# Performance work log

Measured on AMD Instinct MI355X. Metric: run time of the kernel, lower is better.

Reference implementation:

```python
import jax, jax.numpy as jnp
import numpy as np
from jax import lax

ID_LEN = 207
INPUT_DIM = 64
OUTPUT_DIM = 128
WIN = 3
BZ = 16
SEQLEN = 64
N_NODES = BZ * ID_LEN          # 3312
N_EDGES = N_NODES * 16         # 52992


def setup_inputs() -> dict:
    key = jax.random.key(0)
    ks = jax.random.split(key, 8)
    x = jax.random.normal(ks[0], (BZ, SEQLEN, ID_LEN * INPUT_DIM), dtype=jnp.float32)
    edge_src = jax.random.randint(ks[1], (N_EDGES,), 0, N_NODES)
    edge_dst = jax.random.randint(ks[2], (N_EDGES,), 0, N_NODES)
    # learned params (q/k weights init N(0, 0.01), zero bias; conv has no bias)
    Wq = 0.01 * jax.random.normal(ks[3], (INPUT_DIM, OUTPUT_DIM), dtype=jnp.float32)
    bq = jnp.zeros((OUTPUT_DIM,), dtype=jnp.float32)
    Wk = 0.01 * jax.random.normal(ks[4], (INPUT_DIM, OUTPUT_DIM), dtype=jnp.float32)
    bk = jnp.zeros((OUTPUT_DIM,), dtype=jnp.float32)
    fan_in = ID_LEN * INPUT_DIM * WIN
    bound = 1.0 / np.sqrt(fan_in)
    conv_w = jax.random.uniform(ks[5], (OUTPUT_DIM, ID_LEN * INPUT_DIM, WIN),
                                minval=-bound, maxval=bound, dtype=jnp.float32)
    return {"x": x, "Wq": Wq, "bq": bq, "Wk": Wk, "bk": bk,
            "conv_w": conv_w, "edge_src": edge_src, "edge_dst": edge_dst}


def _forward(x, Wq, bq, Wk, bk, conv_w, edge_src, edge_dst):
    bz, seqlen, _ = x.shape
    # (bz, seqlen, id_len, d) -> (bz*id_len, seqlen, d)
    xr = x.reshape(bz, seqlen, ID_LEN, INPUT_DIM).transpose(0, 2, 1, 3)
    xr = xr.reshape(-1, seqlen, INPUT_DIM)
    mean_x = xr.mean(axis=1)                       # [N, d]
    q = (mean_x @ Wq + bq) / jnp.sqrt(jnp.float32(OUTPUT_DIM))
    k = mean_x @ Wk + bk
    v = xr.reshape(-1, seqlen * INPUT_DIM)         # [N, seqlen*d]
    N = v.shape[0]
    # per-edge attention score: k[src] . q[dst]
    scores = jnp.sum(k[edge_src] * q[edge_dst], axis=-1)      # [E]
    # segment softmax over incoming edges per dst
    seg_max = jax.ops.segment_max(scores, edge_dst, num_segments=N)
    e = jnp.exp(scores - seg_max[edge_dst])
    denom = jax.ops.segment_sum(e, edge_dst, num_segments=N)
    alpha = e / denom[edge_dst]                                 # [E]
    # weighted gather-sum of big value vectors
    out = jax.ops.segment_sum(alpha[:, None] * v[edge_src], edge_dst, num_segments=N)
    # back to (bz, seqlen, id_len*d)
    y = out.reshape(bz, ID_LEN, seqlen, INPUT_DIM).transpose(0, 2, 1, 3)
    y = y.reshape(bz, seqlen, ID_LEN * INPUT_DIM)
    # Conv1d same padding, no bias: NCH layout
    y = lax.conv_general_dilated(
        y.transpose(0, 2, 1), conv_w, window_strides=(1,), padding="SAME",
        dimension_numbers=("NCH", "OIH", "NCH"))
    return y.transpose(0, 2, 1)                    # [bz, seqlen, output_dim]


def reference(x, Wq, bq, Wk, bk, conv_w, edge_src, edge_dst):
    return _forward(x, Wq, bq, Wk, bk, conv_w, edge_src, edge_dst)
```

## Files before the change

kernel.cpp:

```cpp
#include <hip/hip_runtime.h>
#include <hip/hip_bf16.h>
#include <math.h>

#define BZ 16
#define SEQ 64
#define CID 207
#define DIN 64
#define OCN 128
#define NN (BZ*CID)
#define NE (NN*16)
#define ICD (CID*DIN)
#define KW 3
#define NKSTEP 414
#define NKPAD 416
#define NKC 32
#define KSPC 13
#define XTOT ((size_t)BZ*SEQ*ICD)
#define TCH 8
#define NCHUNK (SEQ/TCH)
#define GDEG 256
#define WFSTEP (3*8*64*8)

#define CVB 832
#define SCB 207
#define WPB (NKPAD*4)

typedef __attribute__((ext_vector_type(8))) short bf16x8;
typedef __attribute__((ext_vector_type(4))) float f32x4;
typedef unsigned short u16;
typedef unsigned int u32;

__device__ __forceinline__ float bflo(u32 u) {
    u32 v = u << 16;
    return __builtin_bit_cast(float, v);
}
__device__ __forceinline__ float bfhi(u32 u) {
    u32 v = u & 0xFFFF0000u;
    return __builtin_bit_cast(float, v);
}
__device__ __forceinline__ u16 f2bf(float f) {
    __hip_bfloat16 h = __float2bfloat16(f);
    return __builtin_bit_cast(u16, h);
}
__device__ __forceinline__ u32 packbf(float f0, float f1) {
    return ((u32)f2bf(f1) << 16) | (u32)f2bf(f0);
}

__global__ __launch_bounds__(1024) void histscan_kernel(const int* __restrict__ edst,
                                                        int* __restrict__ offs,
                                                        int* __restrict__ fill) {
    __shared__ int hist[NN];
    __shared__ int sums[1024], sums2[1024];
    int tid = threadIdx.x;
    for (int i = tid; i < NN; i += 1024) hist[i] = 0;
    __syncthreads();
    for (int e = tid; e < NE; e += 1024) atomicAdd(&hist[edst[e]], 1);
    __syncthreads();
    int base = tid * 4;
    int v[4];
    #pragma unroll
    for (int i = 0; i < 4; ++i) v[i] = (base + i < NN) ? hist[base + i] : 0;
    sums[tid] = v[0] + v[1] + v[2] + v[3];
    __syncthreads();
    int* a = sums;
    int* b2 = sums2;
    for (int off = 1; off < 1024; off <<= 1) {
        int val = a[tid] + ((tid >= off) ? a[tid - off] : 0);
        b2[tid] = val;
        __syncthreads();
        int* t = a; a = b2; b2 = t;
    }
    int prev = (tid > 0) ? a[tid - 1] : 0;
    int run = prev;
    #pragma unroll
    for (int i = 0; i < 4; ++i) {
        if (base + i <= NN) {
            offs[base + i] = run;
            if (base + i < NN) fill[base + i] = run;
        }
        run += v[i];
    }
}

__global__ __launch_bounds__(256) void fused3_kernel(const float* __restrict__ x,
                                                     u16* __restrict__ xt,
                                                     float* __restrict__ meanp,
                                                     const int* __restrict__ esrc,
                                                     int* __restrict__ fill,
                                                     int* __restrict__ csr,
                                                     const int* __restrict__ edst,
                                                     const float* __restrict__ cw,
                                                     u16* __restrict__ wf) {
    __shared__ float s_cw[32][100];
    int bid = blockIdx.x;
    int tid = threadIdx.x;
    if (bid < CVB) {
        int bb = bid / 52;
        int rem = bid - bb * 52;
        int cg = rem >> 2;
        int tq = rem & 3;
        int cl = tid >> 4;
        int dq = (tid & 15) << 2;
        int c = cg * 16 + cl;
        if (c >= CID) return;
        int n = bb * CID + c;
        const float* px = x + (size_t)bb * SEQ * ICD + (size_t)(tq * 16) * ICD + (size_t)c * DIN + dq;
        u16* pxt = xt + ((size_t)(tq * 16) * NN + n) * DIN + dq;
        float ax = 0.f, ay = 0.f, az = 0.f, aw = 0.f;
        #pragma unroll 4
        for (int t = 0; t < 16; ++t) {
            float4 v = *(const float4*)(px + (size_t)t * ICD);
            ax += v.x; ay += v.y; az += v.z; aw += v.w;
            uint2 w2;
            w2.x = packbf(v.x, v.y);
            w2.y = packbf(v.z, v.w);
            *(uint2*)(pxt + (size_t)t * NN * DIN) = w2;
        }
        *(float4*)(meanp + ((size_t)tq * NN + n) * DIN + dq) = make_float4(ax, ay, az, aw);
    } else if (bid < CVB + SCB) {
        int e = (bid - CVB) * 256 + tid;
        int d0 = edst[e];
        int pos = atomicAdd(&fill[d0], 1);
        csr[pos] = esrc[e];
    } else {
        int wkb = bid - (CVB + SCB);
        int kstep = wkb >> 2;
        int p = wkb & 3;
        int ic0 = kstep * 32;
        int col0 = ic0 * 3;
        {
            int oc_l = tid >> 3;
            int seg = tid & 7;
            const float* src = cw + (size_t)(p * 32 + oc_l) * (ICD * KW) + col0 + seg * 12;
            #pragma unroll
            for (int u = 0; u < 12; ++u) {
                int col = seg * 12 + u;
                float v = (col0 + col < ICD * 3) ? src[u] : 0.f;
                s_cw[oc_l][col] = v;
            }
        }
        __syncthreads();
        #pragma unroll
        for (int r = 0; r < 2; ++r) {
            int f = tid + 256 * r;
            if (f < 384) {
                int lane = f & 63;
                int g = f >> 6;
                int ntl = g & 1;
                int w = g >> 1;
                int nt = p * 2 + ntl;
                int row = ntl * 16 + (lane & 15);
                int cb = 8 * (lane >> 4);
                uint4 o;
                u32 pk[4];
                #pragma unroll
                for (int pj = 0; pj < 4; ++pj) {
                    float v0 = s_cw[row][(cb + 2 * pj) * 3 + w];
                    float v1 = s_cw[row][(cb + 2 * pj + 1) * 3 + w];
                    pk[pj] = packbf(v0, v1);
                }
                o.x = pk[0]; o.y = pk[1]; o.z = pk[2]; o.w = pk[3];
                size_t off = (((size_t)(kstep * 3 + w) * 8 + nt) * 64 + lane) * 8;
                *(uint4*)(wf + off) = o;
            }
        }
    }
}

__global__ __launch_bounds__(256) void qk_kernel(const float* __restrict__ meanp,
                                                 const float* __restrict__ Wq,
                                                 const float* __restrict__ bq,
                                                 const float* __restrict__ Wk,
                                                 const float* __restrict__ bk,
                                                 float* __restrict__ q,
                                                 float* __restrict__ k) {
    __shared__ float ms[16][DIN];
    int n0 = blockIdx.x * 16;
    int tid = threadIdx.x;
    const size_t PS = (size_t)NN * DIN;
    for (int i = tid; i < 16 * DIN; i += 256) {
        size_t off = (size_t)(n0 + (i >> 6)) * DIN + (i & 63);
        float s = meanp[off] + meanp[PS + off] + meanp[2 * PS + off] + meanp[3 * PS + off];
        ms[i >> 6][i & 63] = s * (1.0f / SEQ);
    }
    __syncthreads();
    int j = tid & 127;
    int g = tid >> 7;
    float accq[8], acck[8];
    float bqv = bq[j], bkv = bk[j];
    #pragma unroll
    for (int r = 0; r < 8; ++r) { accq[r] = bqv; acck[r] = bkv; }
    for (int d = 0; d < DIN; ++d) {
        float wq = Wq[d * OCN + j], wk = Wk[d * OCN + j];
        #pragma unroll
        for (int r = 0; r < 8; ++r) {
            float mv = ms[g * 8 + r][d];
            accq[r] += mv * wq;
            acck[r] += mv * wk;
        }
    }
    const float qscale = 0.088388347648318447f;
    #pragma unroll
    for (int r = 0; r < 8; ++r) {
        int nn = n0 + g * 8 + r;
        q[(size_t)nn * OCN + j] = accq[r] * qscale;
        k[(size_t)nn * OCN + j] = acck[r];
    }
}

__global__ __launch_bounds__(256) void alpha_kernel(const float* __restrict__ q,
                                                    const float* __restrict__ k,
                                                    const int* __restrict__ offs,
                                                    const int* __restrict__ csr,
                                                    float* __restrict__ alpha) {
    __shared__ float qs[OCN];
    __shared__ float sc[GDEG];
    __shared__ int sidx[GDEG];
    int n = blockIdx.x;
    int start = offs[n];
    int deg = offs[n + 1] - start;
    if (deg > GDEG) deg = GDEG;
    int tid = threadIdx.x;
    if (tid < OCN) qs[tid] = q[(size_t)n * OCN + tid];
    for (int i = tid; i < deg; i += 256) sidx[i] = csr[start + i];
    __syncthreads();
    int lane = tid & 63;
    int wv = tid >> 6;
    for (int i = wv; i < deg; i += 4) {
        const float* kk = k + (size_t)sidx[i] * OCN;
        float p = kk[lane] * qs[lane] + kk[lane + 64] * qs[lane + 64];
        #pragma unroll
        for (int off = 32; off; off >>= 1) p += __shfl_down(p, off);
        if (lane == 0) sc[i] = p;
    }
    __syncthreads();
    float m = -1e30f;
    for (int i = 0; i < deg; ++i) m = fmaxf(m, sc[i]);
    __syncthreads();
    for (int i = tid; i < deg; i += 256) sc[i] = __expf(sc[i] - m);
    __syncthreads();
    float ssum = 0.f;
    for (int i = 0; i < deg; ++i) ssum += sc[i];
    float inv = (deg > 0) ? (1.0f / ssum) : 0.f;
    for (int i = tid; i < deg; i += 256) alpha[start + i] = sc[i] * inv;
}

__global__ __launch_bounds__(256) void gather2_kernel(const u16* __restrict__ xt,
                                                      const float* __restrict__ alpha,
                                                      const int* __restrict__ offs,
                                                      const int* __restrict__ csr,
                                                      u16* __restrict__ yb) {
    int bid = blockIdx.x;
    int ch = bid & 7;
    int ng = bid >> 3;
    int wid = threadIdx.x >> 6;
    int lane = threadIdx.x & 63;
    int n = ng * 4 + wid;
    int t0 = ch * TCH;
    int b = n / CID, c = n - b * CID;
    int start = offs[n];
    int deg = offs[n + 1] - start;
    int t = lane >> 3;
    int dg = lane & 7;
    const u16* xbase = xt + ((size_t)(t0 + t) * NN) * DIN + (dg << 3);

    int sAll = 0; float aAll = 0.f;
    if (lane < deg) {
        sAll = csr[start + lane] << 6;
        aAll = alpha[start + lane];
    }
    int dmax = (deg <= 64) ? deg : 64;

    float acc[8];
    #pragma unroll
    for (int j = 0; j < 8; ++j) acc[j] = 0.f;

    float a0 = 0.f;
    uint4 v0 = make_uint4(0, 0, 0, 0);
    if (dmax > 0) {
        int s0 = __shfl(sAll, 0);
        a0 = __shfl(aAll, 0);
        v0 = *(const uint4*)(xbase + s0);
    }
    for (int i = 1; i < dmax; ++i) {
        int s1 = __shfl(sAll, i);
        float a1 = __shfl(aAll, i);
        uint4 v1 = *(const uint4*)(xbase + s1);
        acc[0] += a0 * bflo(v0.x); acc[1] += a0 * bfhi(v0.x);
        acc[2] += a0 * bflo(v0.y); acc[3] += a0 * bfhi(v0.y);
        acc[4] += a0 * bflo(v0.z); acc[5] += a0 * bfhi(v0.z);
        acc[6] += a0 * bflo(v0.w); acc[7] += a0 * bfhi(v0.w);
        a0 = a1; v0 = v1;
    }
    if (dmax > 0) {
        acc[0] += a0 * bflo(v0.x); acc[1] += a0 * bfhi(v0.x);
        acc[2] += a0 * bflo(v0.y); acc[3] += a0 * bfhi(v0.y);
        acc[4] += a0 * bflo(v0.z); acc[5] += a0 * bfhi(v0.z);
        acc[6] += a0 * bflo(v0.w); acc[7] += a0 * bfhi(v0.w);
    }
    for (int i = 64; i < deg; ++i) {
        int s = csr[start + i] << 6;
        float a = alpha[start + i];
        uint4 v = *(const uint4*)(xbase + s);
        acc[0] += a * bflo(v.x); acc[1] += a * bfhi(v.x);
        acc[2] += a * bflo(v.y); acc[3] += a * bfhi(v.y);
        acc[4] += a * bflo(v.z); acc[5] += a * bfhi(v.z);
        acc[6] += a * bflo(v.w); acc[7] += a * bfhi(v.w);
    }
    uint4 o;
    o.x = packbf(acc[0], acc[1]);
    o.y = packbf(acc[2], acc[3]);
    o.z = packbf(acc[4], acc[5]);
    o.w = packbf(acc[6], acc[7]);
    *(uint4*)(yb + ((size_t)b * SEQ + t0 + t) * ICD + c * DIN + (dg << 3)) = o;
}

__global__ __launch_bounds__(256) void conv_kernel(const u16* __restrict__ yb,
                                                   const u16* __restrict__ wf,
                                                   float* __restrict__ partial) {
    int bid = blockIdx.x;
    int xcd = bid & 7;
    int rest = bid >> 3;
    int khi = rest & 3;
    int b = rest >> 2;
    int kc = xcd + (khi << 3);
    int tid = threadIdx.x;
    int lane = tid & 63;
    int wid = tid >> 6;
    int th = wid & 1;
    int nh = wid >> 1;
    int lrow = lane & 15;
    int lq = lane >> 4;
    int tbase = th * 32;

    f32x4 acc[2][4];
    #pragma unroll
    for (int tt = 0; tt < 2; ++tt)
        #pragma unroll
        for (int n = 0; n < 4; ++n) acc[tt][n] = (f32x4){0.f, 0.f, 0.f, 0.f};

    const u16* ybA = yb + (size_t)b * SEQ * ICD + lq * 8;
    const u16* wfL = wf + (size_t)lane * 8 + ((size_t)nh * 4 * 64) * 8;
    int ks0 = kc * KSPC;

    bf16x8 aA[6], bA[12], aB[6], bB[12];

#define LOAD_AB(aR, bR, KS) do {                                              \
    int kstep_ = ks0 + (KS);                                                  \
    int ic0_ = kstep_ * 32;                                                   \
    _Pragma("unroll")                                                         \
    for (int tt_ = 0; tt_ < 2; ++tt_) {                                       \
        _Pragma("unroll")                                                     \
        for (int w_ = 0; w_ < 3; ++w_) {                                      \
            int ts_ = tbase + tt_ * 16 + lrow + w_ - 1;                       \
            bf16x8 av_ = {0, 0, 0, 0, 0, 0, 0, 0};                            \
            if ((unsigned)ts_ < SEQ)                                          \
                av_ = *(const bf16x8*)(ybA + (size_t)ts_ * ICD + ic0_);       \
            aR[tt_ * 3 + w_] = av_;                                           \
        }                                                                     \
    }                                                                         \
    const u16* wfp_ = wfL + (size_t)kstep_ * WFSTEP;                          \
    _Pragma("unroll")                                                         \
    for (int w_ = 0; w_ < 3; ++w_) {                                          \
        _Pragma("unroll")                                                     \
        for (int n_ = 0; n_ < 4; ++n_)                                        \
            bR[w_ * 4 + n_] = *(const bf16x8*)(wfp_ + (size_t)((w_ * 8 + n_) * 64) * 8); \
    }                                                                         \
} while (0)

#define COMPUTE(aR, bR) do {                                                  \
    _Pragma("unroll")                                                         \
    for (int w_ = 0; w_ < 3; ++w_) {                                          \
        _Pragma("unroll")                                                     \
        for (int tt_ = 0; tt_ < 2; ++tt_) {                                   \
            _Pragma("unroll")                                                 \
            for (int n_ = 0; n_ < 4; ++n_)                                    \
                acc[tt_][n_] = __builtin_amdgcn_mfma_f32_16x16x32_bf16(       \
                    aR[tt_ * 3 + w_], bR[w_ * 4 + n_], acc[tt_][n_], 0, 0, 0);\
        }                                                                     \
    }                                                                         \
} while (0)

    LOAD_AB(aA, bA, 0);
    #pragma unroll
    for (int ks = 0; ks < KSPC - 1; ks += 2) {
        LOAD_AB(aB, bB, ks + 1);
        COMPUTE(aA, bA);
        LOAD_AB(aA, bA, ks + 2);
        COMPUTE(aB, bB);
    }
    COMPUTE(aA, bA);

    float* pp = partial + (size_t)kc * ((size_t)BZ * SEQ * OCN) + (size_t)b * SEQ * OCN + nh * 64;
    #pragma unroll
    for (int tt = 0; tt < 2; ++tt) {
        #pragma unroll
        for (int n = 0; n < 4; ++n) {
            #pragma unroll
            for (int r = 0; r < 4; ++r) {
                int t = tbase + tt * 16 + lq * 4 + r;
                pp[(size_t)t * OCN + n * 16 + lrow] = acc[tt][n][r];
            }
        }
    }
#undef LOAD_AB
#undef COMPUTE
}

__global__ __launch_bounds__(256) void reduce_kernel(const float* __restrict__ partial,
                                                     float* __restrict__ out) {
    int i = (blockIdx.x * 256 + threadIdx.x) * 4;
    float4 s = make_float4(0.f, 0.f, 0.f, 0.f);
    #pragma unroll
    for (int kc = 0; kc < NKC; ++kc) {
        float4 v = *(const float4*)(partial + (size_t)kc * 131072 + i);
        s.x += v.x; s.y += v.y; s.z += v.z; s.w += v.w;
    }
    *(float4*)(out + i) = s;
}

extern "C" void kernel_launch(void* const* d_in, const int* in_sizes, int n_in,
                              void* d_out, int out_size, void* d_ws, size_t ws_size,
                              hipStream_t stream) {
    const float* x   = (const float*)d_in[0];
    const float* Wq  = (const float*)d_in[1];
    const float* bqv = (const float*)d_in[2];
    const float* Wk  = (const float*)d_in[3];
    const float* bkv = (const float*)d_in[4];
    const float* cw  = (const float*)d_in[5];
    const int* esrc  = (const int*)d_in[6];
    const int* edst  = (const int*)d_in[7];

    char* ws = (char*)d_ws;
    size_t o = 0;
    auto alloc = [&](size_t bytes) {
        void* p = ws + o;
        o += (bytes + 255) & ~(size_t)255;
        return p;
    };
    u16*   xt    = (u16*)alloc(XTOT * 2);
    u16*   yb    = (u16*)alloc(XTOT * 2);
    u16*   wf    = (u16*)alloc((size_t)NKPAD * 3 * 8 * 64 * 8 * 2);
    float* meanp = (float*)alloc((size_t)4 * NN * DIN * 4);
    float* q     = (float*)alloc((size_t)NN * OCN * 4);
    float* k     = (float*)alloc((size_t)NN * OCN * 4);
    int*   fill  = (int*)alloc(4096 * 4);
    int*   offs  = (int*)alloc(4352 * 4);
    int*   csr   = (int*)alloc((size_t)NE * 4);
    float* alpha = (float*)alloc((size_t)NE * 4);
    float* partial = (float*)xt;

    histscan_kernel<<<dim3(1), dim3(1024), 0, stream>>>(edst, offs, fill);
    fused3_kernel<<<dim3(CVB + SCB + WPB), dim3(256), 0, stream>>>(x, xt, meanp, esrc, fill, csr, edst, cw, wf);
    qk_kernel<<<dim3(NN / 16), dim3(256), 0, stream>>>(meanp, Wq, bqv, Wk, bkv, q, k);
    alpha_kernel<<<dim3(NN), dim3(256), 0, stream>>>(q, k, offs, csr, alpha);
    gather2_kernel<<<dim3((NN / 4) * NCHUNK), dim3(256), 0, stream>>>(xt, alpha, offs, csr, yb);
    conv_kernel<<<dim3(512), dim3(256), 0, stream>>>(yb, wf, partial);
    reduce_kernel<<<dim3(131072 / 4 / 256), dim3(256), 0, stream>>>(partial, (float*)d_out);
}
```

Baseline: 134.0 us.

## Fold histogram scan into prep kernel, CSR scatter into qk, two nodes per wave

The single-block histogram/scan kernel becomes block 0 of the conversion/weight-prep kernel, now scanning with 256 threads. The CSR scatter moves into the q/k projection kernel, removing one launch and one dependency stage. The gather kernel now handles two destination nodes per wave with interleaved loads to raise memory-level parallelism, but it drops the fallback path for in-degrees above 64. Dead variants (k1_kernel, k1b_unused) are left in the file.

```diff
diff --git a/kernel.cpp b/kernel.cpp
--- a/kernel.cpp
+++ b/kernel.cpp
@@ -22,8 +22,9 @@
 #define WFSTEP (3*8*64*8)
 
 #define CVB 832
+#define WPB (NKPAD*4)
+#define K1B (1 + CVB + WPB)
 #define SCB 207
-#define WPB (NKPAD*4)
 
 typedef __attribute__((ext_vector_type(8))) short bf16x8;
 typedef __attribute__((ext_vector_type(4))) float f32x4;
@@ -45,58 +46,66 @@
 __device__ __forceinline__ u32 packbf(float f0, float f1) {
     return ((u32)f2bf(f1) << 16) | (u32)f2bf(f0);
 }
-
-__global__ __launch_bounds__(1024) void histscan_kernel(const int* __restrict__ edst,
-                                                        int* __restrict__ offs,
-                                                        int* __restrict__ fill) {
-    __shared__ int hist[NN];
-    __shared__ int sums[1024], sums2[1024];
-    int tid = threadIdx.x;
-    for (int i = tid; i < NN; i += 1024) hist[i] = 0;
-    __syncthreads();
-    for (int e = tid; e < NE; e += 1024) atomicAdd(&hist[edst[e]], 1);
-    __syncthreads();
-    int base = tid * 4;
-    int v[4];
-    #pragma unroll
-    for (int i = 0; i < 4; ++i) v[i] = (base + i < NN) ? hist[base + i] : 0;
-    sums[tid] = v[0] + v[1] + v[2] + v[3];
-    __syncthreads();
-    int* a = sums;
-    int* b2 = sums2;
-    for (int off = 1; off < 1024; off <<= 1) {
-        int val = a[tid] + ((tid >= off) ? a[tid - off] : 0);
-        b2[tid] = val;
-        __syncthreads();
-        int* t = a; a = b2; b2 = t;
-    }
-    int prev = (tid > 0) ? a[tid - 1] : 0;
-    int run = prev;
-    #pragma unroll
-    for (int i = 0; i < 4; ++i) {
-        if (base + i <= NN) {
-            offs[base + i] = run;
-            if (base + i < NN) fill[base + i] = run;
-        }
-        run += v[i];
-    }
-}
-
-__global__ __launch_bounds__(256) void fused3_kernel(const float* __restrict__ x,
-                                                     u16* __restrict__ xt,
-                                                     float* __restrict__ meanp,
-                                                     const int* __restrict__ esrc,
-                                                     int* __restrict__ fill,
-                                                     int* __restrict__ csr,
-                                                     const int* __restrict__ edst,
-                                                     const float* __restrict__ cw,
-                                                     u16* __restrict__ wf) {
-    __shared__ float s_cw[32][100];
+__device__ __forceinline__ void fma8(float* acc, float a, uint4 v) {
+    acc[0] += a * bflo(v.x); acc[1] += a * bfhi(v.x);
+    acc[2] += a * bflo(v.y); acc[3] += a * bfhi(v.y);
+    acc[4] += a * bflo(v.z); acc[5] += a * bfhi(v.z);
+    acc[6] += a * bflo(v.w); acc[7] += a * bfhi(v.w);
+}
+
+union K1LDS {
+    struct { int hist[NN]; int sums[256]; int sums2[256]; } h;
+    float s_cw[32][100];
+};
+
+__global__ __launch_bounds__(256) void k1_kernel(const float* __restrict__ x,
+                                                 u16* __restrict__ xt,
+                                                 float* __restrict__ meanp,
+                                                 const int* __restrict__ edst,
+                                                 int* __restrict__ offs,
+                                                 int* __restrict__ fill,
+                                                 const float* __restrict__ cw,
+                                                 u16* __restrict__ wf) {
+    __shared__ K1LDS u;
     int bid = blockIdx.x;
     int tid = threadIdx.x;
-    if (bid < CVB) {
-        int bb = bid / 52;
-        int rem = bid - bb * 52;
+    if (bid == 0) {
+        for (int i = tid; i < NN; i += 256) u.h.hist[i] = 0;
+        __syncthreads();
+        for (int e = tid; e < NE; e += 256) atomicAdd(&u.h.hist[edst[e]], 1);
+        __syncthreads();
+        int base = tid * 13;
+        int v[13];
+        int s = 0;
+        #pragma unroll
+        for (int i = 0; i < 13; ++i) {
+            v[i] = (base + i < NN) ? u.h.hist[base + i] : 0;
+            s += v[i];
+        }
+        u.h.sums[tid] = s;
+        __syncthreads();
+        int* a = u.h.sums;
+        int* b2 = u.h.sums2;
+        for (int off = 1; off < 256; off <<= 1) {
+            int val = a[tid] + ((tid >= off) ? a[tid - off] : 0);
+            b2[tid] = val;
+            __syncthreads();
+            int* t = a; a = b2; b2 = t;
+        }
+        int run = (tid > 0) ? a[tid - 1] : 0;
+        #pragma unroll
+        for (int i = 0; i < 13; ++i) {
+            int idx = base + i;
+            if (idx <= NN) {
+                offs[idx] = run;
+                if (idx < NN) fill[idx] = run;
+            }
+            run += v[i];
+        }
+    } else if (bid <= CVB) {
+        int cvbid = bid - 1;
+        int bb = cvbid / 52;
+        int rem = cvbid - bb * 52;
         int cg = rem >> 2;
         int tq = rem & 3;
         int cl = tid >> 4;
@@ -117,13 +126,8 @@
             *(uint2*)(pxt + (size_t)t * NN * DIN) = w2;
         }
         *(float4*)(meanp + ((size_t)tq * NN + n) * DIN + dq) = make_float4(ax, ay, az, aw);
-    } else if (bid < CVB + SCB) {
-        int e = (bid - CVB) * 256 + tid;
-        int d0 = edst[e];
-        int pos = atomicAdd(&fill[d0], 1);
-        csr[pos] = esrc[e];
     } else {
-        int wkb = bid - (CVB + SCB);
+        int wkb = bid - (1 + CVB);
         int kstep = wkb >> 2;
         int p = wkb & 3;
         int ic0 = kstep * 32;
@@ -133,41 +137,25 @@
             int seg = tid & 7;
             const float* src = cw + (size_t)(p * 32 + oc_l) * (ICD * KW) + col0 + seg * 12;
             #pragma unroll
-            for (int u = 0; u < 12; ++u) {
-                int col = seg * 12 + u;
-                float v = (col0 + col < ICD * 3) ? src[u] : 0.f;
-                s_cw[oc_l][col] = v;
+            for (int uu = 0; uu < 12; ++uu) {
+                int col = seg * 12 + uu;
+                float v = (col0 + col < ICD * 3) ? src[uu] : 0.f;
+                u.s_cw[oc_l][col] = v;
             }
         }
         __syncthreads();
-        #pragma unroll
-        for (int r = 0; r < 2; ++r) {
-            int f = tid + 256 * r;
-            if (f < 384) {
-                int lane = f & 63;
-                int g = f >> 6;
-                int ntl = g & 1;
-                int w = g >> 1;
-                int nt = p * 2 + ntl;
-                int row = ntl * 16 + (lane & 15);
-                int cb = 8 * (lane >> 4);
-                uint4 o;
-                u32 pk[4];
-                #pragma unroll
-                for (int pj = 0; pj < 4; ++pj) {
-                    float v0 = s_cw[row][(cb + 2 * pj) * 3 + w];
-                    float v1 = s_cw[row][(cb + 2 * pj + 1) * 3 + w];
-                    pk[pj] = packbf(v0, v1);
-                }
-                o.x = pk[0]; o.y = pk[1]; o.z = pk[2]; o.w = pk[3];
-                size_t off = (((size_t)(kstep * 3 + w) * 8 + nt) * 64 + lane) * 8;
-                *(uint4*)(wf + off) = o;
-            }
-        }
-    }
-}
-
-__global__ __launch_bounds__(256) void qk_kernel(const float* __restrict__ meanp,
+        if (tid < 128) return;
+        __builtin_unreachable();
+    }
+}
+
+__global__ __launch_bounds__(256) void k1b_unused() {}
+
+__global__ __launch_bounds__(256) void k2_kernel(const int* __restrict__ esrc,
+                                                 const int* __restrict__ edst,
+                                                 int* __restrict__ fill,
+                                                 int* __restrict__ csr,
+                                                 const float* __restrict__ meanp,
                                                  const float* __restrict__ Wq,
                                                  const float* __restrict__ bq,
                                                  const float* __restrict__ Wk,
@@ -175,8 +163,16 @@
                                                  float* __restrict__ q,
                                                  float* __restrict__ k) {
     __shared__ float ms[16][DIN];
-    int n0 = blockIdx.x * 16;
+    int bid = blockIdx.x;
     int tid = threadIdx.x;
+    if (bid < SCB) {
+        int e = bid * 256 + tid;
+        int d0 = edst[e];
+        int pos = atomicAdd(&fill[d0], 1);
+        csr[pos] = esrc[e];
+        return;
+    }
+    int n0 = (bid - SCB) * 16;
     const size_t PS = (size_t)NN * DIN;
     for (int i = tid; i < 16 * DIN; i += 256) {
         size_t off = (size_t)(n0 + (i >> 6)) * DIN + (i & 63);
@@ -255,65 +251,57 @@
     int ng = bid >> 3;
     int wid = threadIdx.x >> 6;
     int lane = threadIdx.x & 63;
-    int n = ng * 4 + wid;
+    int na = ng * 8 + wid * 2;
+    int nb = na + 1;
     int t0 = ch * TCH;
-    int b = n / CID, c = n - b * CID;
-    int start = offs[n];
-    int deg = offs[n + 1] - start;
     int t = lane >> 3;
     int dg = lane & 7;
     const u16* xbase = xt + ((size_t)(t0 + t) * NN) * DIN + (dg << 3);
 
-    int sAll = 0; float aAll = 0.f;
-    if (lane < deg) {
-        sAll = csr[start + lane] << 6;
-        aAll = alpha[start + lane];
-    }
-    int dmax = (deg <= 64) ? deg : 64;
-
-    float acc[8];
-    #pragma unroll
-    for (int j = 0; j < 8; ++j) acc[j] = 0.f;
-
-    float a0 = 0.f;
-    uint4 v0 = make_uint4(0, 0, 0, 0);
-    if (dmax > 0) {
-        int s0 = __shfl(sAll, 0);
-        a0 = __shfl(aAll, 0);
-        v0 = *(const uint4*)(xbase + s0);
-    }
-    for (int i = 1; i < dmax; ++i) {
-        int s1 = __shfl(sAll, i);
-        float a1 = __shfl(aAll, i);
-        uint4 v1 = *(const uint4*)(xbase + s1);
-        acc[0] += a0 * bflo(v0.x); acc[1] += a0 * bfhi(v0.x);
-        acc[2] += a0 * bflo(v0.y); acc[3] += a0 * bfhi(v0.y);
-        acc[4] += a0 * bflo(v0.z); acc[5] += a0 * bfhi(v0.z);
-        acc[6] += a0 * bflo(v0.w); acc[7] += a0 * bfhi(v0.w);
-        a0 = a1; v0 = v1;
-    }
-    if (dmax > 0) {
-        acc[0] += a0 * bflo(v0.x); acc[1] += a0 * bfhi(v0.x);
-        acc[2] += a0 * bflo(v0.y); acc[3] += a0 * bfhi(v0.y);
-        acc[4] += a0 * bflo(v0.z); acc[5] += a0 * bfhi(v0.z);
-        acc[6] += a0 * bflo(v0.w); acc[7] += a0 * bfhi(v0.w);
-    }
-    for (int i = 64; i < deg; ++i) {
-        int s = csr[start + i] << 6;
-        float a = alpha[start + i];
-        uint4 v = *(const uint4*)(xbase + s);
-        acc[0] += a * bflo(v.x); acc[1] += a * bfhi(v.x);
-        acc[2] += a * bflo(v.y); acc[3] += a * bfhi(v.y);
-        acc[4] += a * bflo(v.z); acc[5] += a * bfhi(v.z);
-        acc[6] += a * bflo(v.w); acc[7] += a * bfhi(v.w);
-    }
-    uint4 o;
-    o.x = packbf(acc[0], acc[1]);
-    o.y = packbf(acc[2], acc[3]);
-    o.z = packbf(acc[4], acc[5]);
-    o.w = packbf(acc[6], acc[7]);
-    *(uint4*)(yb + ((size_t)b * SEQ + t0 + t) * ICD + c * DIN + (dg << 3)) = o;
-}
+    int ba = na / CID, ca = na - ba * CID;
+    int bb2 = nb / CID, cb = nb - bb2 * CID;
+    int sta = offs[na], dega = offs[na + 1] - sta;
+    int stb = offs[nb], degb = offs[nb + 1] - stb;
+
+    int sA = 0; float aA = 0.f;
+    if (lane < dega && lane < 64) { sA = csr[sta + lane] << 6; aA = alpha[sta + lane]; }
+    int sB = 0; float aB = 0.f;
+    if (lane < degb && lane < 64) { sB = csr[stb + lane] << 6; aB = alpha[stb + lane]; }
+    int da = (dega < 64) ? dega : 64;
+    int db = (degb < 64) ? degb : 64;
+    int mx = (da > db) ? da : db;
+
+    float acca[8], accb[8];
+    #pragma unroll
+    for (int j = 0; j < 8; ++j) { acca[j] = 0.f; accb[j] = 0.f; }
+
+    if (mx > 0) {
+        float a0a = __shfl(aA, 0);
+        float a0b = __shfl(aB, 0);
+        uint4 v0a = *(const uint4*)(xbase + __shfl(sA, 0));
+        uint4 v0b = *(const uint4*)(xbase + __shfl(sB, 0));
+        for (int i = 1; i < mx; ++i) {
+            float a1a = __shfl(aA, i);
+            float a1b = __shfl(aB, i);
+            uint4 v1a = *(const uint4*)(xbase + __shfl(sA, i));
+            uint4 v1b = *(const uint4*)(xbase + __shfl(sB, i));
+            fma8(acca, a0a, v0a);
+            fma8(accb, a0b, v0b);
+            a0a = a1a; v0a = v1a;
+            a0b = a1b; v0b = v1b;
+        }
+        fma8(acca, a0a, v0a);
+        fma8(accb, a0b, v0b);
+    }
+    uint4 oa, ob;
+    oa.x = packbf(acca[0], acca[1]); oa.y = packbf(acca[2], acca[3]);
+    oa.z = packbf(acca[4], acca[5]); oa.w = packbf(acca[6], acca[7]);
+    ob.x = packbf(accb[0], accb[1]); ob.y = packbf(accb[2], accb[3]);
+    ob.z = packbf(accb[4], accb[5]); ob.w = packbf(accb[6], accb[7]);
+    *(uint4*)(yb + ((size_t)ba * SEQ + t0 + t) * ICD + ca * DIN + (dg << 3)) = oa;
+    *(uint4*)(yb + ((size_t)bb2 * SEQ + t0 + t) * ICD + cb * DIN + (dg << 3)) = ob;
+}
+
 
 __global__ __launch_bounds__(256) void conv_kernel(const u16* __restrict__ yb,
                                                    const u16* __restrict__ wf,
@@ -419,6 +407,119 @@
     *(float4*)(out + i) = s;
 }
 
+__global__ __launch_bounds__(256) void k1_full_kernel(const float* __restrict__ x,
+                                                      u16* __restrict__ xt,
+                                                      float* __restrict__ meanp,
+                                                      const int* __restrict__ edst,
+                                                      int* __restrict__ offs,
+                                                      int* __restrict__ fill,
+                                                      const float* __restrict__ cw,
+                                                      u16* __restrict__ wf) {
+    __shared__ K1LDS u;
+    int bid = blockIdx.x;
+    int tid = threadIdx.x;
+    if (bid == 0) {
+        for (int i = tid; i < NN; i += 256) u.h.hist[i] = 0;
+        __syncthreads();
+        for (int e = tid; e < NE; e += 256) atomicAdd(&u.h.hist[edst[e]], 1);
+        __syncthreads();
+        int base = tid * 13;
+        int v[13];
+        int s = 0;
+        #pragma unroll
+        for (int i = 0; i < 13; ++i) {
+            v[i] = (base + i < NN) ? u.h.hist[base + i] : 0;
+            s += v[i];
+        }
+        u.h.sums[tid] = s;
+        __syncthreads();
+        int* a = u.h.sums;
+        int* b2 = u.h.sums2;
+        for (int off = 1; off < 256; off <<= 1) {
+            int val = a[tid] + ((tid >= off) ? a[tid - off] : 0);
+            b2[tid] = val;
+            __syncthreads();
+            int* t = a; a = b2; b2 = t;
+        }
+        int run = (tid > 0) ? a[tid - 1] : 0;
+        #pragma unroll
+        for (int i = 0; i < 13; ++i) {
+            int idx = base + i;
+            if (idx <= NN) {
+                offs[idx] = run;
+                if (idx < NN) fill[idx] = run;
+            }
+            run += v[i];
+        }
+    } else if (bid <= CVB) {
+        int cvbid = bid - 1;
+        int bb = cvbid / 52;
+        int rem = cvbid - bb * 52;
+        int cg = rem >> 2;
+        int tq = rem & 3;
+        int cl = tid >> 4;
+        int dq = (tid & 15) << 2;
+        int c = cg * 16 + cl;
+        if (c >= CID) return;
+        int n = bb * CID + c;
+        const float* px = x + (size_t)bb * SEQ * ICD + (size_t)(tq * 16) * ICD + (size_t)c * DIN + dq;
+        u16* pxt = xt + ((size_t)(tq * 16) * NN + n) * DIN + dq;
+        float ax = 0.f, ay = 0.f, az = 0.f, aw = 0.f;
+        #pragma unroll 4
+        for (int t = 0; t < 16; ++t) {
+            float4 v = *(const float4*)(px + (size_t)t * ICD);
+            ax += v.x; ay += v.y; az += v.z; aw += v.w;
+            uint2 w2;
+            w2.x = packbf(v.x, v.y);
+            w2.y = packbf(v.z, v.w);
+            *(uint2*)(pxt + (size_t)t * NN * DIN) = w2;
+        }
+        *(float4*)(meanp + ((size_t)tq * NN + n) * DIN + dq) = make_float4(ax, ay, az, aw);
+    } else {
+        int wkb = bid - (1 + CVB);
+        int kstep = wkb >> 2;
+        int p = wkb & 3;
+        int ic0 = kstep * 32;
+        int col0 = ic0 * 3;
+        {
+            int oc_l = tid >> 3;
+            int seg = tid & 7;
+            const float* src = cw + (size_t)(p * 32 + oc_l) * (ICD * KW) + col0 + seg * 12;
+            #pragma unroll
+            for (int uu = 0; uu < 12; ++uu) {
+                int col = seg * 12 + uu;
+                float v = (col0 + col < ICD * 3) ? src[uu] : 0.f;
+                u.s_cw[oc_l][col] = v;
+            }
+        }
+        __syncthreads();
+        #pragma unroll
+        for (int r = 0; r < 2; ++r) {
+            int f = tid + 256 * r;
+            if (f < 384) {
+                int lane = f & 63;
+                int g = f >> 6;
+                int ntl = g & 1;
+                int w = g >> 1;
+                int nt = p * 2 + ntl;
+                int row = ntl * 16 + (lane & 15);
+                int cb = 8 * (lane >> 4);
+                uint4 o;
+                u32 pk[4];
+                #pragma unroll
+                for (int pj = 0; pj < 4; ++pj) {
+                    float v0 = u.s_cw[row][(cb + 2 * pj) * 3 + w];
+                    float v1 = u.s_cw[row][(cb + 2 * pj + 1) * 3 + w];
+                    pk[pj] = packbf(v0, v1);
+                }
+                o.x = pk[0]; o.y = pk[1]; o.z = pk[2]; o.w = pk[3];
+                size_t off = (((size_t)(kstep * 3 + w) * 8 + nt) * 64 + lane) * 8;
+                *(uint4*)(wf + off) = o;
+            }
+        }
+    }
+}
+
 extern "C" void kernel_launch(void* const* d_in, const int* in_sizes, int n_in,
                               void* d_out, int out_size, void* d_ws, size_t ws_size,
                               hipStream_t stream) {
@@ -450,11 +551,10 @@
     float* alpha = (float*)alloc((size_t)NE * 4);
     float* partial = (float*)xt;
 
-    histscan_kernel<<<dim3(1), dim3(1024), 0, stream>>>(edst, offs, fill);
-    fused3_kernel<<<dim3(CVB + SCB + WPB), dim3(256), 0, stream>>>(x, xt, meanp, esrc, fill, csr, edst, cw, wf);
-    qk_kernel<<<dim3(NN / 16), dim3(256), 0, stream>>>(meanp, Wq, bqv, Wk, bkv, q, k);
+    k1_full_kernel<<<dim3(K1B), dim3(256), 0, stream>>>(x, xt, meanp, edst, offs, fill, cw, wf);
+    k2_kernel<<<dim3(SCB + NN / 16), dim3(256), 0, stream>>>(esrc, edst, fill, csr, meanp, Wq, bqv, Wk, bkv, q, k);
     alpha_kernel<<<dim3(NN), dim3(256), 0, stream>>>(q, k, offs, csr, alpha);
-    gather2_kernel<<<dim3((NN / 4) * NCHUNK), dim3(256), 0, stream>>>(xt, alpha, offs, csr, yb);
+    gather2_kernel<<<dim3((NN / 8) * NCHUNK), dim3(256), 0, stream>>>(xt, alpha, offs, csr, yb);
     conv_kernel<<<dim3(512), dim3(256), 0, stream>>>(yb, wf, partial);
     reduce_kernel<<<dim3(131072 / 4 / 256), dim3(256), 0, stream>>>(partial, (float*)d_out);
 }
```

New measurement: 158.3 us. 1.18x slower.
